# Kernel optimization log

Hardware: AMD Instinct MI355X
Metric: run time of the kernel (lower is better)

The kernel has to match this reference:

```python
import jax, jax.numpy as jnp
import numpy as np

B, S, N, D, H, C, E, DG = 2, 512, 20000, 384, 3, 128, 320000, 128
NEG_SLOPE = 0.2  # PyG GATConv default


def setup_inputs() -> dict:
    key = jax.random.key(0)
    ks = jax.random.split(key, 10)
    p = lambda k, sh: jax.random.normal(k, sh, jnp.float32) * 0.02
    return dict(
        x_enc=jax.random.normal(ks[0], (B, S, D), jnp.float32),
        mask=jax.random.uniform(ks[1], (B, N), dtype=jnp.float32),
        edge_index=jax.random.randint(ks[2], (2, E), 0, N),
        Wq=p(ks[3], (N, S)), bq=jnp.zeros((N,), jnp.float32),
        Wm=p(ks[4], (D, 1)), bm=jnp.zeros((D,), jnp.float32),
        Wlin=p(ks[5], (H * C, D)),
        att_src=p(ks[6], (H, C)), att_dst=p(ks[7], (H, C)),
        bias_gat=jnp.zeros((H * C,), jnp.float32),
        Wproj=p(ks[8], (S, N)), bproj=jnp.zeros((S,), jnp.float32),
        Wtemp=p(ks[9], (DG, H * C)), btemp=jnp.zeros((DG,), jnp.float32),
    )


def reference(x_enc, mask, edge_index, Wq, bq, Wm, bm, Wlin, att_src, att_dst,
              bias_gat, Wproj, bproj, Wtemp, btemp):
    # q = query_proj(x_enc.permute(0,2,1)).permute(0,2,1)  -> [B, N, D]
    q = jnp.einsum('bsd,ns->bnd', x_enc, Wq) + bq[None, :, None]
    # mask_proj: Linear(1, D) on mask[..., None]  -> [B, N, D]
    mask_embed = mask[..., None] * Wm[:, 0] + bm
    x = (q + mask_embed).reshape(B * N, D)

    # batch edge_index with per-graph node offsets, then add self-loops (PyG default)
    offs = (jnp.arange(B, dtype=edge_index.dtype) * N)[:, None]
    src = (edge_index[0][None, :] + offs).reshape(-1)
    dst = (edge_index[1][None, :] + offs).reshape(-1)
    loops = jnp.arange(B * N, dtype=edge_index.dtype)
    src = jnp.concatenate([src, loops])
    dst = jnp.concatenate([dst, loops])

    # GATConv: shared linear, per-head attention
    xp = (x @ Wlin.T).reshape(B * N, H, C)                  # [BN, H, C]
    a_src = jnp.einsum('nhc,hc->nh', xp, att_src)           # [BN, H]
    a_dst = jnp.einsum('nhc,hc->nh', xp, att_dst)
    e = jax.nn.leaky_relu(a_src[src] + a_dst[dst], NEG_SLOPE)  # [Etot, H]
    # segment-softmax over incoming edges of each destination node
    emax = jax.ops.segment_max(e, dst, num_segments=B * N)
    ee = jnp.exp(e - emax[dst])
    denom = jax.ops.segment_sum(ee, dst, num_segments=B * N)
    alpha = ee / denom[dst]                                  # [Etot, H]
    out = jax.ops.segment_sum(xp[src] * alpha[..., None], dst, num_segments=B * N)
    out = out.reshape(B, N, H * C) + bias_gat                # concat heads + bias

    # dropout is identity in eval
    # project: Linear(N, S) over node dim -> [B, S, H*C]
    out = jnp.einsum('bnf,sn->bsf', out, Wproj) + bproj[None, :, None]
    # temp_project: Linear(H*C, d_graph)
    out = out @ Wtemp.T + btemp
    return out
```

## Files before the change

kernel.cpp:

```cpp
#include <hip/hip_runtime.h>
#include <hip/hip_bf16.h>
#include <cstdint>

#define B_   2
#define S_   512
#define N_   20000
#define H_   3
#define C_   128
#define E_   320000
#define DG_  128
#define D_   384
#define BN_  (B_ * N_)
#define F_   (H_ * C_)
#define ETOT_ (B_ * E_ + BN_)

#define MPADQ 20096
#define MPADL 40064

#define PNS2 32
#define PCH2 640

using short8  = __attribute__((ext_vector_type(8))) short;
using floatx4 = __attribute__((ext_vector_type(4))) float;

__device__ __forceinline__ float b2f(unsigned short u) {
  union { unsigned int i; float f; } x; x.i = ((unsigned int)u) << 16; return x.f;
}
__device__ __forceinline__ unsigned short f2b(float f) {
  __hip_bfloat16 b = __float2bfloat16(f);
  return *reinterpret_cast<unsigned short*>(&b);
}

struct bf4 { __hip_bfloat16 a, b, c, d; };

#define NWQ4 ((MPADQ * 512) / 4)
#define NXE4 ((B_ * S_ * D_) / 4)
#define NWL4 ((F_ * D_) / 4)
#define NWP4 ((S_ * N_) / 4)
#define NWT4 ((DG_ * F_) / 4)
#define NCV0 NWQ4
#define NCV1 (NCV0 + NXE4)
#define NCV2 (NCV1 + NWL4)
#define NCV3 (NCV2 + NWP4)
#define NCV4 (NCV3 + NWT4)

__device__ __forceinline__ void cv4(const float* __restrict__ src,
                                    __hip_bfloat16* __restrict__ dst, int e) {
  float4 v = *(const float4*)(src + e);
  bf4 r{__float2bfloat16(v.x), __float2bfloat16(v.y),
        __float2bfloat16(v.z), __float2bfloat16(v.w)};
  *(bf4*)(dst + e) = r;
}

__global__ __launch_bounds__(256) void conv_all_kernel(
    const float* __restrict__ Wq,    __hip_bfloat16* __restrict__ WqB,
    const float* __restrict__ xe,    __hip_bfloat16* __restrict__ xeB,
    const float* __restrict__ Wlin,  __hip_bfloat16* __restrict__ WlinB,
    const float* __restrict__ Wproj, __hip_bfloat16* __restrict__ WprojB,
    const float* __restrict__ Wtemp, __hip_bfloat16* __restrict__ WtempB) {
  int idx = blockIdx.x * 256 + threadIdx.x;
  if (idx < NCV0) {
    int e = idx * 4;
    int row = e >> 9;
    float4 v = make_float4(0.f, 0.f, 0.f, 0.f);
    if (row < N_) v = *(const float4*)(Wq + e);
    bf4 r{__float2bfloat16(v.x), __float2bfloat16(v.y),
          __float2bfloat16(v.z), __float2bfloat16(v.w)};
    *(bf4*)(WqB + e) = r;
  } else if (idx < NCV1) {
    cv4(xe, xeB, (idx - NCV0) * 4);
  } else if (idx < NCV2) {
    cv4(Wlin, WlinB, (idx - NCV1) * 4);
  } else if (idx < NCV3) {
    cv4(Wproj, WprojB, (idx - NCV2) * 4);
  } else if (idx < NCV4) {
    cv4(Wtemp, WtempB, (idx - NCV3) * 4);
  }
}

__global__ __launch_bounds__(256) void prep_epi_kernel(
    const float* __restrict__ Wlin, const float* __restrict__ Wm,
    const float* __restrict__ bm, const float* __restrict__ Wtemp,
    float* __restrict__ epi, float* __restrict__ swt) {
  int w = (blockIdx.x * 256 + threadIdx.x) >> 6;
  int lane = threadIdx.x & 63;
  if (w < F_) {
    float s0 = 0.f, s1 = 0.f, s2 = 0.f;
    const float* row = Wlin + (size_t)w * D_;
    for (int d = lane; d < D_; d += 64) {
      float wv = row[d];
      s0 += wv; s1 += Wm[d] * wv; s2 += bm[d] * wv;
    }
#pragma unroll
    for (int o = 32; o > 0; o >>= 1) {
      s0 += __shfl_down(s0, o); s1 += __shfl_down(s1, o); s2 += __shfl_down(s2, o);
    }
    if (lane == 0) { epi[w] = s0; epi[F_ + w] = s1; epi[2 * F_ + w] = s2; }
  } else if (w < F_ + DG_) {
    int g = w - F_;
    float s = 0.f;
    const float* row = Wtemp + (size_t)g * F_;
    for (int f = lane; f < F_; f += 64) s += row[f];
#pragma unroll
    for (int o = 32; o > 0; o >>= 1) s += __shfl_down(s, o);
    if (lane == 0) swt[g] = s;
  }
}

template <int EPI>
__global__ __launch_bounds__(256) void mfma_gemm_nt(
    const __hip_bfloat16* __restrict__ A, const __hip_bfloat16* __restrict__ Bt,
    __hip_bfloat16* __restrict__ Cout, int K, int Mvalid, int ldc,
    size_t bstrideB, size_t bstrideC,
    const float* __restrict__ bq, const float* __restrict__ mask,
    const float* __restrict__ epi) {
  const int tid = threadIdx.x;
  const int m0 = blockIdx.x * 128;
  const int n0 = blockIdx.y * 128;
  const int bz = blockIdx.z;

  const unsigned short* Ap = (const unsigned short*)A;
  const unsigned short* Bp = (const unsigned short*)(Bt + bstrideB * bz);

  __shared__ __align__(16) unsigned short As[128][40];
  __shared__ __align__(16) unsigned short Bs[128][40];

  const int wave = tid >> 6, lane = tid & 63;
  const int wm = (wave & 1) * 64, wn = (wave >> 1) * 64;
  const int lrow = lane & 15, lk = (lane >> 4) * 8;

  const int srow = tid >> 2;
  const int skoff = (tid & 3) * 8;

  floatx4 acc[4][4];
#pragma unroll
  for (int i = 0; i < 4; ++i)
#pragma unroll
    for (int j = 0; j < 4; ++j) acc[i][j] = floatx4{0.f, 0.f, 0.f, 0.f};

  for (int k0 = 0; k0 < K; k0 += 32) {
    int4 av0 = *(const int4*)(Ap + (size_t)(m0 + srow) * K + k0 + skoff);
    int4 av1 = *(const int4*)(Ap + (size_t)(m0 + 64 + srow) * K + k0 + skoff);
    int4 bv0 = *(const int4*)(Bp + (size_t)(n0 + srow) * K + k0 + skoff);
    int4 bv1 = *(const int4*)(Bp + (size_t)(n0 + 64 + srow) * K + k0 + skoff);
    __syncthreads();
    *(int4*)&As[srow][skoff] = av0;
    *(int4*)&As[64 + srow][skoff] = av1;
    *(int4*)&Bs[srow][skoff] = bv0;
    *(int4*)&Bs[64 + srow][skoff] = bv1;
    __syncthreads();
    short8 af[4], bf[4];
#pragma unroll
    for (int mt = 0; mt < 4; ++mt)
      af[mt] = *(const short8*)&As[wm + mt * 16 + lrow][lk];
#pragma unroll
    for (int nt = 0; nt < 4; ++nt)
      bf[nt] = *(const short8*)&Bs[wn + nt * 16 + lrow][lk];
#pragma unroll
    for (int mt = 0; mt < 4; ++mt)
#pragma unroll
      for (int nt = 0; nt < 4; ++nt)
        acc[mt][nt] = __builtin_amdgcn_mfma_f32_16x16x32_bf16(af[mt], bf[nt],
                                                              acc[mt][nt], 0, 0, 0);
  }

  __hip_bfloat16* Cb = Cout + bstrideC * bz;
#pragma unroll
  for (int mt = 0; mt < 4; ++mt) {
#pragma unroll
    for (int r = 0; r < 4; ++r) {
      int rg = m0 + wm + mt * 16 + (lane >> 4) * 4 + r;
      if (rg < Mvalid) {
        float bqv = 0.f, mkv = 0.f;
        if (EPI) {
          bqv = bq[rg];
          mkv = mask[bz * N_ + rg];
        }
#pragma unroll
        for (int nt = 0; nt < 4; ++nt) {
          int cg = n0 + wn + nt * 16 + lrow;
          float v = acc[mt][nt][r];
          if (EPI) v += bqv * epi[cg] + mkv * epi[F_ + cg] + epi[2 * F_ + cg];
          Cb[(size_t)rg * ldc + cg] = __float2bfloat16(v);
        }
      }
    }
  }
}

__global__ __launch_bounds__(256) void gemm_gn(
    const __hip_bfloat16* __restrict__ A, const __hip_bfloat16* __restrict__ Bt,
    __hip_bfloat16* __restrict__ gnT) {
  const int tid = threadIdx.x;
  const int m0 = blockIdx.x * 128;

  const unsigned short* Ap = (const unsigned short*)A;
  const unsigned short* Bp = (const unsigned short*)Bt;

  __shared__ __align__(16) unsigned short As[128][40];
  __shared__ __align__(16) unsigned short Bs[128][40];

  const int wave = tid >> 6, lane = tid & 63;
  const int wm = (wave & 1) * 64, wn = (wave >> 1) * 64;
  const int lrow = lane & 15, lk = (lane >> 4) * 8;
  const int srow = tid >> 2;
  const int skoff = (tid & 3) * 8;

  floatx4 acc[4][4];
#pragma unroll
  for (int i = 0; i < 4; ++i)
#pragma unroll
    for (int j = 0; j < 4; ++j) acc[i][j] = floatx4{0.f, 0.f, 0.f, 0.f};

  for (int k0 = 0; k0 < F_; k0 += 32) {
    int4 av0 = *(const int4*)(Ap + (size_t)(m0 + srow) * F_ + k0 + skoff);
    int4 av1 = *(const int4*)(Ap + (size_t)(m0 + 64 + srow) * F_ + k0 + skoff);
    int4 bv0 = *(const int4*)(Bp + (size_t)(srow) * F_ + k0 + skoff);
    int4 bv1 = *(const int4*)(Bp + (size_t)(64 + srow) * F_ + k0 + skoff);
    __syncthreads();
    *(int4*)&As[srow][skoff] = av0;
    *(int4*)&As[64 + srow][skoff] = av1;
    *(int4*)&Bs[srow][skoff] = bv0;
    *(int4*)&Bs[64 + srow][skoff] = bv1;
    __syncthreads();
    short8 af[4], bf[4];
#pragma unroll
    for (int mt = 0; mt < 4; ++mt)
      af[mt] = *(const short8*)&As[wm + mt * 16 + lrow][lk];
#pragma unroll
    for (int nt = 0; nt < 4; ++nt)
      bf[nt] = *(const short8*)&Bs[wn + nt * 16 + lrow][lk];
#pragma unroll
    for (int mt = 0; mt < 4; ++mt)
#pragma unroll
      for (int nt = 0; nt < 4; ++nt)
        acc[mt][nt] = __builtin_amdgcn_mfma_f32_16x16x32_bf16(af[mt], bf[nt],
                                                              acc[mt][nt], 0, 0, 0);
  }

#pragma unroll
  for (int mt = 0; mt < 4; ++mt) {
    int rg0 = m0 + wm + mt * 16 + (lane >> 4) * 4;
    if (rg0 < BN_) {
      int b = (rg0 >= N_) ? 1 : 0;
      int n = rg0 - b * N_;
#pragma unroll
      for (int nt = 0; nt < 4; ++nt) {
        int cg = wn + nt * 16 + lrow;
        ushort4 o;
        o.x = f2b(acc[mt][nt][0]); o.y = f2b(acc[mt][nt][1]);
        o.z = f2b(acc[mt][nt][2]); o.w = f2b(acc[mt][nt][3]);
        *(ushort4*)((unsigned short*)gnT + (size_t)b * DG_ * N_ + (size_t)cg * N_ + n) = o;
      }
    }
  }
}

__global__ __launch_bounds__(256) void gemm_proj2(
    const __hip_bfloat16* __restrict__ A, const __hip_bfloat16* __restrict__ Bt,
    float* __restrict__ Ppart) {
  const int tid = threadIdx.x;
  const int m0 = blockIdx.x * 128;
  const int bz = blockIdx.z;
  const int b = bz / PNS2, ks = bz - b * PNS2;
  const int kbeg = ks * PCH2;
  const int kend = (kbeg + PCH2 < N_) ? (kbeg + PCH2) : N_;

  const unsigned short* Ap = (const unsigned short*)A;
  const unsigned short* Bp = (const unsigned short*)(Bt + (size_t)b * DG_ * N_);

  __shared__ __align__(16) unsigned short As[128][40];
  __shared__ __align__(16) unsigned short Bs[128][40];

  const int wave = tid >> 6, lane = tid & 63;
  const int wm = (wave & 1) * 64, wn = (wave >> 1) * 64;
  const int lrow = lane & 15, lk = (lane >> 4) * 8;
  const int srow = tid >> 2;
  const int skoff = (tid & 3) * 8;

  floatx4 acc[4][4];
#pragma unroll
  for (int i = 0; i < 4; ++i)
#pragma unroll
    for (int j = 0; j < 4; ++j) acc[i][j] = floatx4{0.f, 0.f, 0.f, 0.f};

  for (int k0 = kbeg; k0 < kend; k0 += 32) {
    int4 av0 = *(const int4*)(Ap + (size_t)(m0 + srow) * N_ + k0 + skoff);
    int4 av1 = *(const int4*)(Ap + (size_t)(m0 + 64 + srow) * N_ + k0 + skoff);
    int4 bv0 = *(const int4*)(Bp + (size_t)(srow) * N_ + k0 + skoff);
    int4 bv1 = *(const int4*)(Bp + (size_t)(64 + srow) * N_ + k0 + skoff);
    __syncthreads();
    *(int4*)&As[srow][skoff] = av0;
    *(int4*)&As[64 + srow][skoff] = av1;
    *(int4*)&Bs[srow][skoff] = bv0;
    *(int4*)&Bs[64 + srow][skoff] = bv1;
    __syncthreads();
    short8 af[4], bf[4];
#pragma unroll
    for (int mt = 0; mt < 4; ++mt)
      af[mt] = *(const short8*)&As[wm + mt * 16 + lrow][lk];
#pragma unroll
    for (int nt = 0; nt < 4; ++nt)
      bf[nt] = *(const short8*)&Bs[wn + nt * 16 + lrow][lk];
#pragma unroll
    for (int mt = 0; mt < 4; ++mt)
#pragma unroll
      for (int nt = 0; nt < 4; ++nt)
        acc[mt][nt] = __builtin_amdgcn_mfma_f32_16x16x32_bf16(af[mt], bf[nt],
                                                              acc[mt][nt], 0, 0, 0);
  }

  float* Pp = Ppart + (size_t)bz * S_ * DG_;
#pragma unroll
  for (int mt = 0; mt < 4; ++mt) {
#pragma unroll
    for (int r = 0; r < 4; ++r) {
      int rg = m0 + wm + mt * 16 + (lane >> 4) * 4 + r;
#pragma unroll
      for (int nt = 0; nt < 4; ++nt) {
        int cg = wn + nt * 16 + lrow;
        Pp[(size_t)rg * DG_ + cg] = acc[mt][nt][r];
      }
    }
  }
}

__global__ __launch_bounds__(256) void att_kernel(
    const __hip_bfloat16* __restrict__ xp, const float* __restrict__ att_src,
    const float* __restrict__ att_dst, float* __restrict__ a_src,
    float* __restrict__ a_dst) {
  int gid = blockIdx.x * blockDim.x + threadIdx.x;
  int wid = gid >> 6;
  int lane = threadIdx.x & 63;
  if (wid >= BN_ * H_) return;
  int i = wid / H_, h = wid - i * H_;
  const __hip_bfloat16* row = xp + (size_t)i * F_ + h * C_;
  const float* as = att_src + h * C_;
  const float* ad = att_dst + h * C_;
  float v0 = __bfloat162float(row[lane]), v1 = __bfloat162float(row[lane + 64]);
  float s1 = v0 * as[lane] + v1 * as[lane + 64];
  float s2 = v0 * ad[lane] + v1 * ad[lane + 64];
#pragma unroll
  for (int off = 32; off > 0; off >>= 1) {
    s1 += __shfl_down(s1, off);
    s2 += __shfl_down(s2, off);
  }
  if (lane == 0) {
    a_src[i * H_ + h] = s1;
    a_dst[i * H_ + h] = s2;
  }
}

__global__ __launch_bounds__(256) void count_kernel(const int* __restrict__ ei,
                                                    int* __restrict__ counts,
                                                    int* __restrict__ rank) {
  int idx = blockIdx.x * blockDim.x + threadIdx.x;
  if (idx >= 2 * E_) return;
  int b = (idx >= E_) ? 1 : 0;
  int e = idx - b * E_;
  int d = ei[E_ + e];
  rank[idx] = atomicAdd(&counts[b * N_ + d], 1);
}

#define SCB 1024
#define NSCB ((BN_ + SCB - 1) / SCB)
__global__ __launch_bounds__(1024) void scan1_kernel(const int* __restrict__ counts,
                                                     int* __restrict__ offs,
                                                     int* __restrict__ btot) {
  __shared__ int wsum[16];
  int t = threadIdx.x, wave = t >> 6, lane = t & 63;
  int i = blockIdx.x * SCB + t;
  int v = (i < BN_) ? (counts[i] + 1) : 0;
  int x = v;
#pragma unroll
  for (int o = 1; o < 64; o <<= 1) {
    int y = __shfl_up(x, o);
    if (lane >= o) x += y;
  }
  if (lane == 63) wsum[wave] = x;
  __syncthreads();
  if (wave == 0) {
    int w = (lane < 16) ? wsum[lane] : 0;
#pragma unroll
    for (int o = 1; o < 16; o <<= 1) {
      int y = __shfl_up(w, o);
      if (lane >= o) w += y;
    }
    if (lane < 16) wsum[lane] = w;
  }
  __syncthreads();
  int woff = (wave == 0) ? 0 : wsum[wave - 1];
  if (i < BN_) offs[i] = woff + x - v;
  if (t == 0) btot[blockIdx.x] = wsum[15];
}

__global__ __launch_bounds__(64) void scan2_kernel(int* __restrict__ btot) {
  int lane = threadIdx.x;
  int v = (lane < NSCB) ? btot[lane] : 0;
  int x = v;
#pragma unroll
  for (int o = 1; o < 64; o <<= 1) {
    int y = __shfl_up(x, o);
    if (lane >= o) x += y;
  }
  if (lane < NSCB) btot[lane] = x - v;
}

__global__ __launch_bounds__(256) void scan3_kernel(int* __restrict__ offs,
                                                    const int* __restrict__ btot) {
  int i = blockIdx.x * 256 + threadIdx.x;
  if (i < BN_) offs[i] += btot[i >> 10];
}

__global__ __launch_bounds__(256) void fill_kernel(
    const int* __restrict__ ei, const int* __restrict__ rank,
    const int* __restrict__ offs, const int* __restrict__ counts,
    int* __restrict__ col) {
  int idx = blockIdx.x * blockDim.x + threadIdx.x;
  if (idx >= ETOT_) return;
  if (idx < 2 * E_) {
    int b = (idx >= E_) ? 1 : 0;
    int e = idx - b * E_;
    int sg = b * N_ + ei[e];
    int dg = b * N_ + ei[E_ + e];
    col[offs[dg] + rank[idx]] = sg;
  } else {
    int i = idx - 2 * E_;
    col[offs[i] + counts[i]] = i;
  }
}

__global__ __launch_bounds__(256) void denom_kernel(
    const int* __restrict__ offs, const int* __restrict__ counts,
    const int* __restrict__ col, const float* __restrict__ a_src,
    const float* __restrict__ a_dst, float4* __restrict__ rden4,
    float4* __restrict__ sexp4) {
  int i = (blockIdx.x * 256 + threadIdx.x) >> 6;
  int lane = threadIdx.x & 63;
  if (i >= BN_) return;
  int beg = offs[i], nE = counts[i] + 1;
  float ad0 = a_dst[i * 3 + 0], ad1 = a_dst[i * 3 + 1], ad2 = a_dst[i * 3 + 2];
  float d0 = 0.f, d1 = 0.f, d2 = 0.f;
  for (int j = lane; j < nE; j += 64) {
    int s = col[beg + j];
    float e0 = a_src[s * 3 + 0] + ad0;
    float e1 = a_src[s * 3 + 1] + ad1;
    float e2 = a_src[s * 3 + 2] + ad2;
    e0 = (e0 > 0.f) ? e0 : 0.2f * e0;
    e1 = (e1 > 0.f) ? e1 : 0.2f * e1;
    e2 = (e2 > 0.f) ? e2 : 0.2f * e2;
    float x0 = __expf(e0), x1 = __expf(e1), x2 = __expf(e2);
    sexp4[beg + j] = make_float4(x0, x1, x2, 0.f);
    d0 += x0; d1 += x1; d2 += x2;
  }
#pragma unroll
  for (int o = 32; o > 0; o >>= 1) {
    d0 += __shfl_down(d0, o);
    d1 += __shfl_down(d1, o);
    d2 += __shfl_down(d2, o);
  }
  if (lane == 0) rden4[i] = make_float4(1.0f / d0, 1.0f / d1, 1.0f / d2, 0.f);
}

__global__ __launch_bounds__(128) void agg_kernel(
    const int* __restrict__ offs, const int* __restrict__ counts,
    const int* __restrict__ col, const float* __restrict__ sexpw,
    const float4* __restrict__ rden4, const __hip_bfloat16* __restrict__ xp,
    const float* __restrict__ bias_gat, __hip_bfloat16* __restrict__ out) {
  int i = blockIdx.x;
  int t = threadIdx.x;
  if (t >= 96) return;
  int beg = offs[i];
  int nE = counts[i] + 1;

  const ushort4* xp4 = (const ushort4*)xp;
  int h = t >> 5;
  float ax = 0.f, ay = 0.f, az = 0.f, aw = 0.f;

  int j = 0;
  for (; j + 4 <= nE; j += 4) {
    int s0 = col[beg + j + 0], s1 = col[beg + j + 1];
    int s2 = col[beg + j + 2], s3 = col[beg + j + 3];
    float w0 = sexpw[(beg + j + 0) * 4 + h];
    float w1 = sexpw[(beg + j + 1) * 4 + h];
    float w2 = sexpw[(beg + j + 2) * 4 + h];
    float w3 = sexpw[(beg + j + 3) * 4 + h];
    ushort4 v0 = xp4[(size_t)s0 * 96 + t];
    ushort4 v1 = xp4[(size_t)s1 * 96 + t];
    ushort4 v2 = xp4[(size_t)s2 * 96 + t];
    ushort4 v3 = xp4[(size_t)s3 * 96 + t];
    ax = fmaf(w0, b2f(v0.x), ax); ay = fmaf(w0, b2f(v0.y), ay);
    az = fmaf(w0, b2f(v0.z), az); aw = fmaf(w0, b2f(v0.w), aw);
    ax = fmaf(w1, b2f(v1.x), ax); ay = fmaf(w1, b2f(v1.y), ay);
    az = fmaf(w1, b2f(v1.z), az); aw = fmaf(w1, b2f(v1.w), aw);
    ax = fmaf(w2, b2f(v2.x), ax); ay = fmaf(w2, b2f(v2.y), ay);
    az = fmaf(w2, b2f(v2.z), az); aw = fmaf(w2, b2f(v2.w), aw);
    ax = fmaf(w3, b2f(v3.x), ax); ay = fmaf(w3, b2f(v3.y), ay);
    az = fmaf(w3, b2f(v3.z), az); aw = fmaf(w3, b2f(v3.w), aw);
  }
  for (; j < nE; ++j) {
    int s0 = col[beg + j];
    float w0 = sexpw[(beg + j) * 4 + h];
    ushort4 v0 = xp4[(size_t)s0 * 96 + t];
    ax = fmaf(w0, b2f(v0.x), ax); ay = fmaf(w0, b2f(v0.y), ay);
    az = fmaf(w0, b2f(v0.z), az); aw = fmaf(w0, b2f(v0.w), aw);
  }

  float4 rd = rden4[i];
  float r = (h == 0) ? rd.x : ((h == 1) ? rd.y : rd.z);
  const float4 bg = *(const float4*)(bias_gat + t * 4);
  ushort4 o;
  o.x = f2b(ax * r + bg.x);
  o.y = f2b(ay * r + bg.y);
  o.z = f2b(az * r + bg.z);
  o.w = f2b(aw * r + bg.w);
  *(ushort4*)((unsigned short*)out + (size_t)i * F_ + t * 4) = o;
}

__global__ __launch_bounds__(128) void final_kernel(
    const float* __restrict__ Ppart, const float* __restrict__ bproj,
    const float* __restrict__ swt, const float* __restrict__ btemp,
    float* __restrict__ out) {
  int bs = blockIdx.x;
  int b = bs >> 9;
  int s = bs & (S_ - 1);
  int g = threadIdx.x;
  float acc = btemp[g] + bproj[s] * swt[g];
  const float* pp = Ppart + ((size_t)b * PNS2 * S_ + s) * DG_ + g;
  for (int ns = 0; ns < PNS2; ++ns) acc += pp[(size_t)ns * S_ * DG_];
  out[(size_t)bs * DG_ + g] = acc;
}

extern "C" void kernel_launch(void* const* d_in, const int* in_sizes, int n_in,
                              void* d_out, int out_size, void* d_ws, size_t ws_size,
                              hipStream_t stream) {
  const float* x_enc   = (const float*)d_in[0];
  const float* mask    = (const float*)d_in[1];
  const int*   ei      = (const int*)d_in[2];
  const float* Wq      = (const float*)d_in[3];
  const float* bq      = (const float*)d_in[4];
  const float* Wm      = (const float*)d_in[5];
  const float* bm      = (const float*)d_in[6];
  const float* Wlin    = (const float*)d_in[7];
  const float* att_src = (const float*)d_in[8];
  const float* att_dst = (const float*)d_in[9];
  const float* bias_gat= (const float*)d_in[10];
  const float* Wproj   = (const float*)d_in[11];
  const float* bproj   = (const float*)d_in[12];
  const float* Wtemp   = (const float*)d_in[13];
  const float* btemp   = (const float*)d_in[14];
  float* outp = (float*)d_out;

  char* ws = (char*)d_ws;
  size_t off = 0;
  auto alloc = [&](size_t bytes) {
    char* p = ws + off;
    off = (off + bytes + 255) & ~(size_t)255;
    return p;
  };

  const size_t GNT_OFF = (size_t)B_ * PNS2 * S_ * DG_ * 4;
  char* regionA = alloc(GNT_OFF + (size_t)B_ * DG_ * N_ * 2);
  __hip_bfloat16* Wq_b = (__hip_bfloat16*)regionA;
  float* Ppart = (float*)regionA;
  __hip_bfloat16* gnT  = (__hip_bfloat16*)(regionA + GNT_OFF);

  __hip_bfloat16* xeB    = (__hip_bfloat16*)alloc((size_t)B_ * S_ * D_ * 2);
  __hip_bfloat16* yT     = (__hip_bfloat16*)alloc((size_t)B_ * F_ * S_ * 2);
  __hip_bfloat16* xp     = (__hip_bfloat16*)alloc((size_t)BN_ * F_ * 2);
  __hip_bfloat16* gat    = (__hip_bfloat16*)alloc((size_t)MPADL * F_ * 2);
  __hip_bfloat16* WlinB  = (__hip_bfloat16*)alloc((size_t)F_ * D_ * 2);
  __hip_bfloat16* WprojB = (__hip_bfloat16*)alloc((size_t)S_ * N_ * 2);
  __hip_bfloat16* WtempB = (__hip_bfloat16*)alloc((size_t)DG_ * F_ * 2);
  float* epi   = (float*)alloc((size_t)3 * F_ * 4);
  float* swt   = (float*)alloc((size_t)DG_ * 4);
  float* a_src = (float*)alloc((size_t)BN_ * H_ * 4);
  float* a_dst = (float*)alloc((size_t)BN_ * H_ * 4);
  int* counts  = (int*)alloc((size_t)BN_ * 4);
  int* offsb   = (int*)alloc((size_t)BN_ * 4);
  int* rank    = (int*)alloc((size_t)2 * E_ * 4);
  int* col     = (int*)alloc((size_t)ETOT_ * 4);
  int* btot    = (int*)alloc((size_t)NSCB * 4);
  float4* rden4 = (float4*)alloc((size_t)BN_ * 16);
  float4* sexp4 = (float4*)alloc((size_t)ETOT_ * 16);
  if (off > ws_size) return;

  hipMemsetAsync(counts, 0, (size_t)BN_ * 4, stream);
  hipMemsetAsync(gat + (size_t)BN_ * F_, 0, (size_t)(MPADL - BN_) * F_ * 2, stream);

  count_kernel<<<(2 * E_ + 255) / 256, 256, 0, stream>>>(ei, counts, rank);
  scan1_kernel<<<NSCB, SCB, 0, stream>>>(counts, offsb, btot);
  scan2_kernel<<<1, 64, 0, stream>>>(btot);
  scan3_kernel<<<(BN_ + 255) / 256, 256, 0, stream>>>(offsb, btot);
  fill_kernel<<<(ETOT_ + 255) / 256, 256, 0, stream>>>(ei, rank, offsb, counts, col);

  conv_all_kernel<<<(NCV4 + 255) / 256, 256, 0, stream>>>(
      Wq, Wq_b, x_enc, xeB, Wlin, WlinB, Wproj, WprojB, Wtemp, WtempB);
  prep_epi_kernel<<<((F_ + DG_) * 64) / 256, 256, 0, stream>>>(Wlin, Wm, bm, Wtemp, epi, swt);

  mfma_gemm_nt<0><<<dim3(F_ / 128, S_ / 128, B_), 256, 0, stream>>>(
      WlinB, xeB, yT, D_, F_, S_, (size_t)S_ * D_, (size_t)F_ * S_,
      nullptr, nullptr, nullptr);
  mfma_gemm_nt<1><<<dim3(MPADQ / 128, F_ / 128, B_), 256, 0, stream>>>(
      Wq_b, yT, xp, S_, N_, F_, (size_t)F_ * S_, (size_t)N_ * F_,
      bq, mask, epi);

  att_kernel<<<(BN_ * H_ + 3) / 4, 256, 0, stream>>>(xp, att_src, att_dst, a_src, a_dst);
  denom_kernel<<<BN_ / 4, 256, 0, stream>>>(offsb, counts, col, a_src, a_dst, rden4, sexp4);
  agg_kernel<<<BN_, 128, 0, stream>>>(offsb, counts, col, (const float*)sexp4, rden4,
                                      xp, bias_gat, gat);

  gemm_gn<<<dim3(MPADL / 128, 1, 1), 256, 0, stream>>>(gat, WtempB, gnT);
  gemm_proj2<<<dim3(S_ / 128, 1, B_ * PNS2), 256, 0, stream>>>(WprojB, gnT, Ppart);
  final_kernel<<<B_ * S_, 128, 0, stream>>>(Ppart, bproj, swt, btemp, outp);
}
```

Before: 387.1 us.

## Share CSR across batches and fuse softmax denominator into aggregation

Builds the destination-sorted CSR once for a single graph and reuses it for both batch copies, replacing the three-kernel scan with a single-block scan. The separate denominator kernel and its per-edge exp buffer are removed. Aggregation now recomputes leaky-relu/exp per edge and normalizes at the end, with one block handling the same node in both batches. The weight-prep reductions are merged into the conversion kernel to save a launch. Edge exps are now computed redundantly by 32 threads per head instead of stored once.

```diff
diff --git a/kernel.cpp b/kernel.cpp
--- a/kernel.cpp
+++ b/kernel.cpp
@@ -12,7 +12,7 @@
 #define D_   384
 #define BN_  (B_ * N_)
 #define F_   (H_ * C_)
-#define ETOT_ (B_ * E_ + BN_)
+#define ECSR_ (E_ + N_)
 
 #define MPADQ 20096
 #define MPADL 40064
@@ -43,6 +43,7 @@
 #define NCV2 (NCV1 + NWL4)
 #define NCV3 (NCV2 + NWP4)
 #define NCV4 (NCV3 + NWT4)
+#define NCVTOT (NCV4 + (F_ + DG_) * 64)
 
 __device__ __forceinline__ void cv4(const float* __restrict__ src,
                                     __hip_bfloat16* __restrict__ dst, int e) {
@@ -57,7 +58,9 @@
     const float* __restrict__ xe,    __hip_bfloat16* __restrict__ xeB,
     const float* __restrict__ Wlin,  __hip_bfloat16* __restrict__ WlinB,
     const float* __restrict__ Wproj, __hip_bfloat16* __restrict__ WprojB,
-    const float* __restrict__ Wtemp, __hip_bfloat16* __restrict__ WtempB) {
+    const float* __restrict__ Wtemp, __hip_bfloat16* __restrict__ WtempB,
+    const float* __restrict__ Wm,    const float* __restrict__ bm,
+    float* __restrict__ epi,         float* __restrict__ swt) {
   int idx = blockIdx.x * 256 + threadIdx.x;
   if (idx < NCV0) {
     int e = idx * 4;
@@ -75,35 +78,30 @@
     cv4(Wproj, WprojB, (idx - NCV2) * 4);
   } else if (idx < NCV4) {
     cv4(Wtemp, WtempB, (idx - NCV3) * 4);
-  }
-}
-
-__global__ __launch_bounds__(256) void prep_epi_kernel(
-    const float* __restrict__ Wlin, const float* __restrict__ Wm,
-    const float* __restrict__ bm, const float* __restrict__ Wtemp,
-    float* __restrict__ epi, float* __restrict__ swt) {
-  int w = (blockIdx.x * 256 + threadIdx.x) >> 6;
-  int lane = threadIdx.x & 63;
-  if (w < F_) {
-    float s0 = 0.f, s1 = 0.f, s2 = 0.f;
-    const float* row = Wlin + (size_t)w * D_;
-    for (int d = lane; d < D_; d += 64) {
-      float wv = row[d];
-      s0 += wv; s1 += Wm[d] * wv; s2 += bm[d] * wv;
+  } else {
+    int w = (idx - NCV4) >> 6;
+    int lane = idx & 63;
+    if (w < F_) {
+      float s0 = 0.f, s1 = 0.f, s2 = 0.f;
+      const float* row = Wlin + (size_t)w * D_;
+      for (int d = lane; d < D_; d += 64) {
+        float wv = row[d];
+        s0 += wv; s1 += Wm[d] * wv; s2 += bm[d] * wv;
+      }
+#pragma unroll
+      for (int o = 32; o > 0; o >>= 1) {
+        s0 += __shfl_down(s0, o); s1 += __shfl_down(s1, o); s2 += __shfl_down(s2, o);
+      }
+      if (lane == 0) { epi[w] = s0; epi[F_ + w] = s1; epi[2 * F_ + w] = s2; }
+    } else {
+      int g = w - F_;
+      float s = 0.f;
+      const float* row = Wtemp + (size_t)g * F_;
+      for (int f = lane; f < F_; f += 64) s += row[f];
+#pragma unroll
+      for (int o = 32; o > 0; o >>= 1) s += __shfl_down(s, o);
+      if (lane == 0) swt[g] = s;
     }
-#pragma unroll
-    for (int o = 32; o > 0; o >>= 1) {
-      s0 += __shfl_down(s0, o); s1 += __shfl_down(s1, o); s2 += __shfl_down(s2, o);
-    }
-    if (lane == 0) { epi[w] = s0; epi[F_ + w] = s1; epi[2 * F_ + w] = s2; }
-  } else if (w < F_ + DG_) {
-    int g = w - F_;
-    float s = 0.f;
-    const float* row = Wtemp + (size_t)g * F_;
-    for (int f = lane; f < F_; f += 64) s += row[f];
-#pragma unroll
-    for (int o = 32; o > 0; o >>= 1) s += __shfl_down(s, o);
-    if (lane == 0) swt[g] = s;
   }
 }
 
@@ -355,61 +353,47 @@
                                                     int* __restrict__ counts,
                                                     int* __restrict__ rank) {
   int idx = blockIdx.x * blockDim.x + threadIdx.x;
-  if (idx >= 2 * E_) return;
-  int b = (idx >= E_) ? 1 : 0;
-  int e = idx - b * E_;
-  int d = ei[E_ + e];
-  rank[idx] = atomicAdd(&counts[b * N_ + d], 1);
-}
-
-#define SCB 1024
-#define NSCB ((BN_ + SCB - 1) / SCB)
-__global__ __launch_bounds__(1024) void scan1_kernel(const int* __restrict__ counts,
-                                                     int* __restrict__ offs,
-                                                     int* __restrict__ btot) {
+  if (idx >= E_) return;
+  int d = ei[E_ + idx];
+  rank[idx] = atomicAdd(&counts[d], 1);
+}
+
+__global__ __launch_bounds__(1024) void scan_kernel(const int* __restrict__ counts,
+                                                    int* __restrict__ offs) {
   __shared__ int wsum[16];
+  __shared__ int carry;
   int t = threadIdx.x, wave = t >> 6, lane = t & 63;
-  int i = blockIdx.x * SCB + t;
-  int v = (i < BN_) ? (counts[i] + 1) : 0;
-  int x = v;
-#pragma unroll
-  for (int o = 1; o < 64; o <<= 1) {
-    int y = __shfl_up(x, o);
-    if (lane >= o) x += y;
-  }
-  if (lane == 63) wsum[wave] = x;
+  if (t == 0) carry = 0;
   __syncthreads();
-  if (wave == 0) {
-    int w = (lane < 16) ? wsum[lane] : 0;
-#pragma unroll
-    for (int o = 1; o < 16; o <<= 1) {
-      int y = __shfl_up(w, o);
-      if (lane >= o) w += y;
+  for (int base = 0; base < N_; base += 1024) {
+    int i = base + t;
+    int v = (i < N_) ? (counts[i] + 1) : 0;
+    int x = v;
+#pragma unroll
+    for (int o = 1; o < 64; o <<= 1) {
+      int y = __shfl_up(x, o);
+      if (lane >= o) x += y;
     }
-    if (lane < 16) wsum[lane] = w;
-  }
-  __syncthreads();
-  int woff = (wave == 0) ? 0 : wsum[wave - 1];
-  if (i < BN_) offs[i] = woff + x - v;
-  if (t == 0) btot[blockIdx.x] = wsum[15];
-}
-
-__global__ __launch_bounds__(64) void scan2_kernel(int* __restrict__ btot) {
-  int lane = threadIdx.x;
-  int v = (lane < NSCB) ? btot[lane] : 0;
-  int x = v;
-#pragma unroll
-  for (int o = 1; o < 64; o <<= 1) {
-    int y = __shfl_up(x, o);
-    if (lane >= o) x += y;
-  }
-  if (lane < NSCB) btot[lane] = x - v;
-}
-
-__global__ __launch_bounds__(256) void scan3_kernel(int* __restrict__ offs,
-                                                    const int* __restrict__ btot) {
-  int i = blockIdx.x * 256 + threadIdx.x;
-  if (i < BN_) offs[i] += btot[i >> 10];
+    if (lane == 63) wsum[wave] = x;
+    __syncthreads();
+    int c = carry;
+    if (wave == 0) {
+      int w = (lane < 16) ? wsum[lane] : 0;
+#pragma unroll
+      for (int o = 1; o < 16; o <<= 1) {
+        int y = __shfl_up(w, o);
+        if (lane >= o) w += y;
+      }
+      if (lane < 16) wsum[lane] = w;
+    }
+    __syncthreads();
+    int woff = (wave == 0) ? 0 : wsum[wave - 1];
+    int excl = c + woff + x - v;
+    if (i < N_) offs[i] = excl;
+    int total = wsum[15];
+    __syncthreads();
+    if (t == 0) carry = c + total;
+  }
 }
 
 __global__ __launch_bounds__(256) void fill_kernel(
@@ -417,78 +401,57 @@
     const int* __restrict__ offs, const int* __restrict__ counts,
     int* __restrict__ col) {
   int idx = blockIdx.x * blockDim.x + threadIdx.x;
-  if (idx >= ETOT_) return;
-  if (idx < 2 * E_) {
-    int b = (idx >= E_) ? 1 : 0;
-    int e = idx - b * E_;
-    int sg = b * N_ + ei[e];
-    int dg = b * N_ + ei[E_ + e];
+  if (idx >= ECSR_) return;
+  if (idx < E_) {
+    int sg = ei[idx];
+    int dg = ei[E_ + idx];
     col[offs[dg] + rank[idx]] = sg;
   } else {
-    int i = idx - 2 * E_;
-    col[offs[i] + counts[i]] = i;
-  }
-}
-
-__global__ __launch_bounds__(256) void denom_kernel(
+    int n = idx - E_;
+    col[offs[n] + counts[n]] = n;
+  }
+}
+
+__global__ __launch_bounds__(192) void agg_kernel(
     const int* __restrict__ offs, const int* __restrict__ counts,
     const int* __restrict__ col, const float* __restrict__ a_src,
-    const float* __restrict__ a_dst, float4* __restrict__ rden4,
-    float4* __restrict__ sexp4) {
-  int i = (blockIdx.x * 256 + threadIdx.x) >> 6;
-  int lane = threadIdx.x & 63;
-  if (i >= BN_) return;
-  int beg = offs[i], nE = counts[i] + 1;
-  float ad0 = a_dst[i * 3 + 0], ad1 = a_dst[i * 3 + 1], ad2 = a_dst[i * 3 + 2];
-  float d0 = 0.f, d1 = 0.f, d2 = 0.f;
-  for (int j = lane; j < nE; j += 64) {
-    int s = col[beg + j];
-    float e0 = a_src[s * 3 + 0] + ad0;
-    float e1 = a_src[s * 3 + 1] + ad1;
-    float e2 = a_src[s * 3 + 2] + ad2;
+    const float* __restrict__ a_dst, const __hip_bfloat16* __restrict__ xp,
+    const float* __restrict__ bias_gat, __hip_bfloat16* __restrict__ out) {
+  int n = blockIdx.x;
+  int t = threadIdx.x;
+  int q = (t >= 96) ? 1 : 0;
+  int tt = t - q * 96;
+  int qn = q * N_;
+  int i = qn + n;
+  int beg = offs[n];
+  int nE = counts[n] + 1;
+  int h = tt >> 5;
+
+  const ushort4* xp4 = (const ushort4*)xp;
+  float ad = a_dst[(size_t)i * 3 + h];
+  float ax = 0.f, ay = 0.f, az = 0.f, aw = 0.f, sw = 0.f;
+
+  int j = 0;
+  for (; j + 4 <= nE; j += 4) {
+    int s0 = col[beg + j + 0] + qn;
+    int s1 = col[beg + j + 1] + qn;
+    int s2 = col[beg + j + 2] + qn;
+    int s3 = col[beg + j + 3] + qn;
+    float e0 = a_src[(size_t)s0 * 3 + h] + ad;
+    float e1 = a_src[(size_t)s1 * 3 + h] + ad;
+    float e2 = a_src[(size_t)s2 * 3 + h] + ad;
+    float e3 = a_src[(size_t)s3 * 3 + h] + ad;
     e0 = (e0 > 0.f) ? e0 : 0.2f * e0;
     e1 = (e1 > 0.f) ? e1 : 0.2f * e1;
     e2 = (e2 > 0.f) ? e2 : 0.2f * e2;
-    float x0 = __expf(e0), x1 = __expf(e1), x2 = __expf(e2);
-    sexp4[beg + j] = make_float4(x0, x1, x2, 0.f);
-    d0 += x0; d1 += x1; d2 += x2;
-  }
-#pragma unroll
-  for (int o = 32; o > 0; o >>= 1) {
-    d0 += __shfl_down(d0, o);
-    d1 += __shfl_down(d1, o);
-    d2 += __shfl_down(d2, o);
-  }
-  if (lane == 0) rden4[i] = make_float4(1.0f / d0, 1.0f / d1, 1.0f / d2, 0.f);
-}
-
-__global__ __launch_bounds__(128) void agg_kernel(
-    const int* __restrict__ offs, const int* __restrict__ counts,
-    const int* __restrict__ col, const float* __restrict__ sexpw,
-    const float4* __restrict__ rden4, const __hip_bfloat16* __restrict__ xp,
-    const float* __restrict__ bias_gat, __hip_bfloat16* __restrict__ out) {
-  int i = blockIdx.x;
-  int t = threadIdx.x;
-  if (t >= 96) return;
-  int beg = offs[i];
-  int nE = counts[i] + 1;
-
-  const ushort4* xp4 = (const ushort4*)xp;
-  int h = t >> 5;
-  float ax = 0.f, ay = 0.f, az = 0.f, aw = 0.f;
-
-  int j = 0;
-  for (; j + 4 <= nE; j += 4) {
-    int s0 = col[beg + j + 0], s1 = col[beg + j + 1];
-    int s2 = col[beg + j + 2], s3 = col[beg + j + 3];
-    float w0 = sexpw[(beg + j + 0) * 4 + h];
-    float w1 = sexpw[(beg + j + 1) * 4 + h];
-    float w2 = sexpw[(beg + j + 2) * 4 + h];
-    float w3 = sexpw[(beg + j + 3) * 4 + h];
-    ushort4 v0 = xp4[(size_t)s0 * 96 + t];
-    ushort4 v1 = xp4[(size_t)s1 * 96 + t];
-    ushort4 v2 = xp4[(size_t)s2 * 96 + t];
-    ushort4 v3 = xp4[(size_t)s3 * 96 + t];
+    e3 = (e3 > 0.f) ? e3 : 0.2f * e3;
+    float w0 = __expf(e0), w1 = __expf(e1);
+    float w2 = __expf(e2), w3 = __expf(e3);
+    sw += (w0 + w1) + (w2 + w3);
+    ushort4 v0 = xp4[(size_t)s0 * 96 + tt];
+    ushort4 v1 = xp4[(size_t)s1 * 96 + tt];
+    ushort4 v2 = xp4[(size_t)s2 * 96 + tt];
+    ushort4 v3 = xp4[(size_t)s3 * 96 + tt];
     ax = fmaf(w0, b2f(v0.x), ax); ay = fmaf(w0, b2f(v0.y), ay);
     az = fmaf(w0, b2f(v0.z), az); aw = fmaf(w0, b2f(v0.w), aw);
     ax = fmaf(w1, b2f(v1.x), ax); ay = fmaf(w1, b2f(v1.y), ay);
@@ -499,22 +462,24 @@
     az = fmaf(w3, b2f(v3.z), az); aw = fmaf(w3, b2f(v3.w), aw);
   }
   for (; j < nE; ++j) {
-    int s0 = col[beg + j];
-    float w0 = sexpw[(beg + j) * 4 + h];
-    ushort4 v0 = xp4[(size_t)s0 * 96 + t];
+    int s0 = col[beg + j] + qn;
+    float e0 = a_src[(size_t)s0 * 3 + h] + ad;
+    e0 = (e0 > 0.f) ? e0 : 0.2f * e0;
+    float w0 = __expf(e0);
+    sw += w0;
+    ushort4 v0 = xp4[(size_t)s0 * 96 + tt];
     ax = fmaf(w0, b2f(v0.x), ax); ay = fmaf(w0, b2f(v0.y), ay);
     az = fmaf(w0, b2f(v0.z), az); aw = fmaf(w0, b2f(v0.w), aw);
   }
 
-  float4 rd = rden4[i];
-  float r = (h == 0) ? rd.x : ((h == 1) ? rd.y : rd.z);
-  const float4 bg = *(const float4*)(bias_gat + t * 4);
+  float r = 1.0f / sw;
+  const float4 bg = *(const float4*)(bias_gat + tt * 4);
   ushort4 o;
   o.x = f2b(ax * r + bg.x);
   o.y = f2b(ay * r + bg.y);
   o.z = f2b(az * r + bg.z);
   o.w = f2b(aw * r + bg.w);
-  *(ushort4*)((unsigned short*)out + (size_t)i * F_ + t * 4) = o;
+  *(ushort4*)((unsigned short*)out + (size_t)i * F_ + tt * 4) = o;
 }
 
 __global__ __launch_bounds__(128) void final_kernel(
@@ -576,27 +541,22 @@
   float* swt   = (float*)alloc((size_t)DG_ * 4);
   float* a_src = (float*)alloc((size_t)BN_ * H_ * 4);
   float* a_dst = (float*)alloc((size_t)BN_ * H_ * 4);
-  int* counts  = (int*)alloc((size_t)BN_ * 4);
-  int* offsb   = (int*)alloc((size_t)BN_ * 4);
-  int* rank    = (int*)alloc((size_t)2 * E_ * 4);
-  int* col     = (int*)alloc((size_t)ETOT_ * 4);
-  int* btot    = (int*)alloc((size_t)NSCB * 4);
-  float4* rden4 = (float4*)alloc((size_t)BN_ * 16);
-  float4* sexp4 = (float4*)alloc((size_t)ETOT_ * 16);
+  int* counts  = (int*)alloc((size_t)N_ * 4);
+  int* offsb   = (int*)alloc((size_t)N_ * 4);
+  int* rank    = (int*)alloc((size_t)E_ * 4);
+  int* col     = (int*)alloc((size_t)ECSR_ * 4);
   if (off > ws_size) return;
 
-  hipMemsetAsync(counts, 0, (size_t)BN_ * 4, stream);
+  hipMemsetAsync(counts, 0, (size_t)N_ * 4, stream);
   hipMemsetAsync(gat + (size_t)BN_ * F_, 0, (size_t)(MPADL - BN_) * F_ * 2, stream);
 
-  count_kernel<<<(2 * E_ + 255) / 256, 256, 0, stream>>>(ei, counts, rank);
-  scan1_kernel<<<NSCB, SCB, 0, stream>>>(counts, offsb, btot);
-  scan2_kernel<<<1, 64, 0, stream>>>(btot);
-  scan3_kernel<<<(BN_ + 255) / 256, 256, 0, stream>>>(offsb, btot);
-  fill_kernel<<<(ETOT_ + 255) / 256, 256, 0, stream>>>(ei, rank, offsb, counts, col);
-
-  conv_all_kernel<<<(NCV4 + 255) / 256, 256, 0, stream>>>(
-      Wq, Wq_b, x_enc, xeB, Wlin, WlinB, Wproj, WprojB, Wtemp, WtempB);
-  prep_epi_kernel<<<((F_ + DG_) * 64) / 256, 256, 0, stream>>>(Wlin, Wm, bm, Wtemp, epi, swt);
+  count_kernel<<<(E_ + 255) / 256, 256, 0, stream>>>(ei, counts, rank);
+  scan_kernel<<<1, 1024, 0, stream>>>(counts, offsb);
+  fill_kernel<<<(ECSR_ + 255) / 256, 256, 0, stream>>>(ei, rank, offsb, counts, col);
+
+  conv_all_kernel<<<NCVTOT / 256, 256, 0, stream>>>(
+      Wq, Wq_b, x_enc, xeB, Wlin, WlinB, Wproj, WprojB, Wtemp, WtempB,
+      Wm, bm, epi, swt);
 
   mfma_gemm_nt<0><<<dim3(F_ / 128, S_ / 128, B_), 256, 0, stream>>>(
       WlinB, xeB, yT, D_, F_, S_, (size_t)S_ * D_, (size_t)F_ * S_,
@@ -606,9 +566,8 @@
       bq, mask, epi);
 
   att_kernel<<<(BN_ * H_ + 3) / 4, 256, 0, stream>>>(xp, att_src, att_dst, a_src, a_dst);
-  denom_kernel<<<BN_ / 4, 256, 0, stream>>>(offsb, counts, col, a_src, a_dst, rden4, sexp4);
-  agg_kernel<<<BN_, 128, 0, stream>>>(offsb, counts, col, (const float*)sexp4, rden4,
-                                      xp, bias_gat, gat);
+  agg_kernel<<<N_, 192, 0, stream>>>(offsb, counts, col, a_src, a_dst,
+                                     xp, bias_gat, gat);
 
   gemm_gn<<<dim3(MPADL / 128, 1, 1), 256, 0, stream>>>(gat, WtempB, gnT);
   gemm_proj2<<<dim3(S_ / 128, 1, B_ * PNS2), 256, 0, stream>>>(WprojB, gnT, Ppart);
```

Result: faster. 374.6 us (-3.2%).
